# Optimization experiments

Measured on AMD Instinct MI355X. Metric: run time of the kernel, lower is better.

Reference implementation:

```python
import jax, jax.numpy as jnp
import numpy as np

N = 50000   # n_nodes (cells)
E = 800000  # n_edges (avg degree 16)
D = 128     # feature dim


def setup_inputs() -> dict:
    key = jax.random.key(0)
    ks = jax.random.split(key, 8)
    x = jax.random.normal(ks[0], (N, D), dtype=jnp.float32)
    src = jax.random.randint(ks[1], (E,), 0, N, dtype=jnp.int32)
    dst = jax.random.randint(ks[2], (E,), 0, N, dtype=jnp.int32)
    vals = jax.random.uniform(ks[3], (E,), dtype=jnp.float32)
    # GraphConvolution weight (dim -> dim), applied as x @ W
    W_gc = jax.random.normal(ks[4], (D, D), dtype=jnp.float32) / np.sqrt(D).astype(np.float32)
    b_gc = jnp.zeros((D,), jnp.float32)
    # linear2: nn.Linear(dim, dim) -> x @ W2.T + b2
    W2 = jax.random.normal(ks[5], (D, D), dtype=jnp.float32) / np.sqrt(D).astype(np.float32)
    b2 = jnp.zeros((D,), jnp.float32)
    return {"x": x, "vals": vals, "W_gc": W_gc, "b_gc": b_gc,
            "W2": W2, "b2": b2, "src": src, "dst": dst}


def reference(x, vals, W_gc, b_gc, W2, b2, src, dst):
    # GraphConvolution (dropout is identity in eval mode):
    #   support = x @ W + b ; out = relu(adj_sparse @ support)
    support = x @ W_gc + b_gc                         # [N, D]
    msg = support[src] * vals[:, None]                # gather rows, scale by edge weight
    agg = jax.ops.segment_sum(msg, dst, num_segments=N)  # SpMM via scatter-add
    x1 = jax.nn.relu(agg)                             # [N, D]
    # linear2 + dropout(eval=identity) + detached L2 row-normalize
    x2 = x1 @ W2.T + b2                               # [N, D]
    nrm = jax.lax.stop_gradient(
        jnp.sqrt(jnp.sum(x2 * x2, axis=1, keepdims=True)))
    return x2 / nrm
```

## Files before the change

### kernel.cpp

```cpp
#include <hip/hip_runtime.h>
#include <hip/hip_bf16.h>

#define N_NODES 50000
#define N_EDGES 800000
#define DIM     128
#define N_STRIPS (N_NODES / 16)
#define N_BKT    782
#define EDGE_CHUNKS 196
#define BCAP     1536
#define EBUF_CAP 1408
#define AGS      68
#define GEMM_BLOCKS ((N_STRIPS + 3) / 4)
#define FRONT_BLOCKS (GEMM_BLOCKS + EDGE_CHUNKS)

typedef short short8 __attribute__((ext_vector_type(8)));
typedef float floatx4 __attribute__((ext_vector_type(4)));

__device__ inline unsigned short f2bf(float f) {
    __hip_bfloat16 h = __float2bfloat16(f);
    return *reinterpret_cast<unsigned short*>(&h);
}

__global__ __launch_bounds__(256) void pre_pack(
    const float* __restrict__ W1, const float* __restrict__ W2,
    uint4* __restrict__ p1, uint4* __restrict__ p2, int* __restrict__ bcnt)
{
    const int blk = blockIdx.x;
    const int t   = threadIdx.x;
    if (blk < 8) {
        const int s    = blk * 256 + t;
        const int lane = s & 63;
        const int nt   = (s >> 6) & 7;
        const int ks   = s >> 9;
        const int m    = lane & 15;
        const int q    = lane >> 4;
        unsigned short e[8];
        #pragma unroll
        for (int j = 0; j < 8; ++j)
            e[j] = f2bf(W1[(ks * 32 + q * 8 + j) * DIM + nt * 16 + m]);
        uint4 o;
        o.x = (unsigned)e[0] | ((unsigned)e[1] << 16);
        o.y = (unsigned)e[2] | ((unsigned)e[3] << 16);
        o.z = (unsigned)e[4] | ((unsigned)e[5] << 16);
        o.w = (unsigned)e[6] | ((unsigned)e[7] << 16);
        p1[s] = o;
    } else if (blk < 16) {
        const int s    = (blk - 8) * 256 + t;
        const int lane = s & 63;
        const int nt   = (s >> 6) & 7;
        const int ks   = s >> 9;
        const int m    = lane & 15;
        const int q    = lane >> 4;
        const float4 f0 = *reinterpret_cast<const float4*>(&W2[(nt * 16 + m) * DIM + ks * 32 + q * 8]);
        const float4 f1 = *reinterpret_cast<const float4*>(&W2[(nt * 16 + m) * DIM + ks * 32 + q * 8 + 4]);
        unsigned short e[8];
        e[0] = f2bf(f0.x); e[1] = f2bf(f0.y); e[2] = f2bf(f0.z); e[3] = f2bf(f0.w);
        e[4] = f2bf(f1.x); e[5] = f2bf(f1.y); e[6] = f2bf(f1.z); e[7] = f2bf(f1.w);
        uint4 o;
        o.x = (unsigned)e[0] | ((unsigned)e[1] << 16);
        o.y = (unsigned)e[2] | ((unsigned)e[3] << 16);
        o.z = (unsigned)e[4] | ((unsigned)e[5] << 16);
        o.w = (unsigned)e[6] | ((unsigned)e[7] << 16);
        p2[s] = o;
    } else {
        for (int i = t; i < 800; i += 256) bcnt[i] = 0;
    }
}

__global__ __launch_bounds__(256) void front(
    const float* __restrict__ x, const float* __restrict__ bias,
    const int* __restrict__ src, const int* __restrict__ dst,
    const float* __restrict__ vals, const uint4* __restrict__ p1,
    unsigned short* __restrict__ support, int* __restrict__ bcnt,
    int2* __restrict__ bucketed)
{
    __shared__ int bh[800];
    __shared__ int rcur[800];
    const int t = threadIdx.x;

    if (blockIdx.x < EDGE_CHUNKS) {
        const int chunk = blockIdx.x;
        for (int i = t; i < 800; i += 256) bh[i] = 0;
        __syncthreads();
        const int base   = chunk * 4096;
        const int navail = min(4096, N_EDGES - base);
        const int4* d4 = reinterpret_cast<const int4*>(dst + base);
        #pragma unroll
        for (int i = 0; i < 4; ++i) {
            const int j = t + i * 256;
            if (j * 4 < navail) {
                const int4 d = d4[j];
                atomicAdd(&bh[d.x >> 6], 1);
                atomicAdd(&bh[d.y >> 6], 1);
                atomicAdd(&bh[d.z >> 6], 1);
                atomicAdd(&bh[d.w >> 6], 1);
            }
        }
        __syncthreads();
        for (int b = t; b < N_BKT; b += 256)
            rcur[b] = b * BCAP + atomicAdd(&bcnt[b], bh[b]);
        __syncthreads();
        const int4*   s4 = reinterpret_cast<const int4*>(src + base);
        const float4* v4 = reinterpret_cast<const float4*>(vals + base);
        #pragma unroll
        for (int i = 0; i < 4; ++i) {
            const int j = t + i * 256;
            if (j * 4 < navail) {
                const int4   s = s4[j];
                const int4   d = d4[j];
                const float4 v = v4[j];
                int p;
                p = atomicAdd(&rcur[d.x >> 6], 1);
                bucketed[p] = make_int2((s.x & 0xFFFF) | ((d.x & 63) << 16), __float_as_int(v.x));
                p = atomicAdd(&rcur[d.y >> 6], 1);
                bucketed[p] = make_int2((s.y & 0xFFFF) | ((d.y & 63) << 16), __float_as_int(v.y));
                p = atomicAdd(&rcur[d.z >> 6], 1);
                bucketed[p] = make_int2((s.z & 0xFFFF) | ((d.z & 63) << 16), __float_as_int(v.z));
                p = atomicAdd(&rcur[d.w >> 6], 1);
                bucketed[p] = make_int2((s.w & 0xFFFF) | ((d.w & 63) << 16), __float_as_int(v.w));
            }
        }
    } else {
        const int wave  = t >> 6;
        const int lane  = t & 63;
        const int strip = (blockIdx.x - EDGE_CHUNKS) * 4 + wave;
        if (strip >= N_STRIPS) return;
        const int m = lane & 15;
        const int q = lane >> 4;
        const int row = strip * 16 + m;

        short8 a[4];
        const float4* xr = reinterpret_cast<const float4*>(&x[(size_t)row * DIM]);
        #pragma unroll
        for (int ks = 0; ks < 4; ++ks) {
            const float4 f0 = xr[ks * 8 + q * 2];
            const float4 f1 = xr[ks * 8 + q * 2 + 1];
            short8 tt;
            tt[0] = (short)f2bf(f0.x); tt[1] = (short)f2bf(f0.y);
            tt[2] = (short)f2bf(f0.z); tt[3] = (short)f2bf(f0.w);
            tt[4] = (short)f2bf(f1.x); tt[5] = (short)f2bf(f1.y);
            tt[6] = (short)f2bf(f1.z); tt[7] = (short)f2bf(f1.w);
            a[ks] = tt;
        }

        floatx4 acc[8];
        #pragma unroll
        for (int nt = 0; nt < 8; ++nt) { acc[nt][0]=0.f; acc[nt][1]=0.f; acc[nt][2]=0.f; acc[nt][3]=0.f; }

        const short8* Bp = (const short8*)p1;
        #pragma unroll
        for (int ks = 0; ks < 4; ++ks) {
            #pragma unroll
            for (int nt = 0; nt < 8; ++nt) {
                const short8 bf = Bp[(ks * 8 + nt) * 64 + lane];
                acc[nt] = __builtin_amdgcn_mfma_f32_16x16x32_bf16(a[ks], bf, acc[nt], 0, 0, 0);
            }
        }

        #pragma unroll
        for (int nt = 0; nt < 8; ++nt) {
            const float bb = bias[nt * 16 + m];
            #pragma unroll
            for (int i = 0; i < 4; ++i) {
                const int r = strip * 16 + q * 4 + i;
                support[(size_t)r * DIM + nt * 16 + m] = f2bf(acc[nt][i] + bb);
            }
        }
    }
}

__global__ __launch_bounds__(256) void agg_gemm2(
    const unsigned int* __restrict__ sup, const int2* __restrict__ bucketed,
    const int* __restrict__ bcnt, const short8* __restrict__ Bp,
    const float* __restrict__ bias, float* __restrict__ out)
{
    __shared__ int2 ebuf[EBUF_CAP];
    __shared__ unsigned int agg[64 * AGS];
    __shared__ int cnt[64];
    __shared__ int coff[64];
    __shared__ int cur[64];

    const int b = blockIdx.x;
    const int t = threadIdx.x;
    int nE = bcnt[b];
    if (nE > EBUF_CAP) nE = EBUF_CAP;
    const int base = b * BCAP;

    if (t < 64) cnt[t] = 0;
    __syncthreads();
    for (int i = t; i < nE; i += 256)
        atomicAdd(&cnt[(bucketed[base + i].x >> 16) & 63], 1);
    __syncthreads();
    if (t < 64) coff[t] = cnt[t];
    __syncthreads();
    for (int off = 1; off < 64; off <<= 1) {
        int u = 0;
        if (t < 64 && t >= off) u = coff[t - off];
        __syncthreads();
        if (t < 64 && t >= off) coff[t] += u;
        __syncthreads();
    }
    if (t < 64) cur[t] = coff[t] - cnt[t];
    __syncthreads();
    for (int i = t; i < nE; i += 256) {
        const int2 e = bucketed[base + i];
        const int  n = (e.x >> 16) & 63;
        const int  p = atomicAdd(&cur[n], 1);
        ebuf[p] = e;
    }
    __syncthreads();

    const int w    = t >> 6;
    const int lane = t & 63;
    const int g    = lane >> 4;
    const int dl   = lane & 15;

    for (int nl = w * 16; nl < w * 16 + 16; ++nl) {
        const int end = cur[nl];
        const int c   = cnt[nl];
        const int beg = end - c;
        float acc[8];
        #pragma unroll
        for (int k = 0; k < 8; ++k) acc[k] = 0.f;

        const int nI = (c + 3) >> 2;
        auto step = [&](int it) {
            const int  idx = beg + it * 4 + g;
            const bool vld = idx < end;
            const int2 e   = ebuf[vld ? idx : beg];
            const float val = vld ? __int_as_float(e.y) : 0.f;
            const uint4 u = *reinterpret_cast<const uint4*>(
                &sup[(size_t)(e.x & 0xFFFF) * 64 + dl * 4]);
            acc[0] += __uint_as_float(u.x << 16)          * val;
            acc[1] += __uint_as_float(u.x & 0xffff0000u)  * val;
            acc[2] += __uint_as_float(u.y << 16)          * val;
            acc[3] += __uint_as_float(u.y & 0xffff0000u)  * val;
            acc[4] += __uint_as_float(u.z << 16)          * val;
            acc[5] += __uint_as_float(u.z & 0xffff0000u)  * val;
            acc[6] += __uint_as_float(u.w << 16)          * val;
            acc[7] += __uint_as_float(u.w & 0xffff0000u)  * val;
        };
        int it = 0;
        for (; it + 3 < nI; it += 4) { step(it); step(it+1); step(it+2); step(it+3); }
        for (; it < nI; ++it) step(it);

        #pragma unroll
        for (int k = 0; k < 8; ++k) {
            acc[k] += __shfl_xor(acc[k], 16);
            acc[k] += __shfl_xor(acc[k], 32);
        }
        if (dl == lane) {
            uint4 o;
            o.x = (unsigned)f2bf(fmaxf(acc[0],0.f)) | ((unsigned)f2bf(fmaxf(acc[1],0.f)) << 16);
            o.y = (unsigned)f2bf(fmaxf(acc[2],0.f)) | ((unsigned)f2bf(fmaxf(acc[3],0.f)) << 16);
            o.z = (unsigned)f2bf(fmaxf(acc[4],0.f)) | ((unsigned)f2bf(fmaxf(acc[5],0.f)) << 16);
            o.w = (unsigned)f2bf(fmaxf(acc[6],0.f)) | ((unsigned)f2bf(fmaxf(acc[7],0.f)) << 16);
            *reinterpret_cast<uint4*>(&agg[nl * AGS + dl * 4]) = o;
        }
    }
    __syncthreads();

    const int row0 = b * 64 + w * 16;
    if (row0 >= N_NODES) return;
    const int m = lane & 15;
    const int q = lane >> 4;

    short8 a[4];
    #pragma unroll
    for (int ks = 0; ks < 4; ++ks) {
        const uint4 t4 = *reinterpret_cast<const uint4*>(&agg[(w * 16 + m) * AGS + ks * 16 + q * 4]);
        a[ks] = *reinterpret_cast<const short8*>(&t4);
    }

    floatx4 acc[8];
    #pragma unroll
    for (int nt = 0; nt < 8; ++nt) { acc[nt][0]=0.f; acc[nt][1]=0.f; acc[nt][2]=0.f; acc[nt][3]=0.f; }

    #pragma unroll
    for (int ks = 0; ks < 4; ++ks) {
        #pragma unroll
        for (int nt = 0; nt < 8; ++nt) {
            const short8 bf = Bp[(ks * 8 + nt) * 64 + lane];
            acc[nt] = __builtin_amdgcn_mfma_f32_16x16x32_bf16(a[ks], bf, acc[nt], 0, 0, 0);
        }
    }

    #pragma unroll
    for (int nt = 0; nt < 8; ++nt) {
        const float bb = bias[nt * 16 + m];
        #pragma unroll
        for (int i = 0; i < 4; ++i) acc[nt][i] += bb;
    }

    float sq[4] = {0.f, 0.f, 0.f, 0.f};
    #pragma unroll
    for (int nt = 0; nt < 8; ++nt)
        #pragma unroll
        for (int i = 0; i < 4; ++i) sq[i] += acc[nt][i] * acc[nt][i];
    #pragma unroll
    for (int i = 0; i < 4; ++i) {
        #pragma unroll
        for (int mask = 1; mask < 16; mask <<= 1)
            sq[i] += __shfl_xor(sq[i], mask);
        sq[i] = 1.0f / sqrtf(sq[i]);
    }

    #pragma unroll
    for (int nt = 0; nt < 8; ++nt) {
        #pragma unroll
        for (int i = 0; i < 4; ++i) {
            const int r = row0 + q * 4 + i;
            out[(size_t)r * DIM + nt * 16 + m] = acc[nt][i] * sq[i];
        }
    }
}

extern "C" void kernel_launch(void* const* d_in, const int* in_sizes, int n_in,
                              void* d_out, int out_size, void* d_ws, size_t ws_size,
                              hipStream_t stream) {
    const float* x    = (const float*)d_in[0];
    const float* vals = (const float*)d_in[1];
    const float* W_gc = (const float*)d_in[2];
    const float* b_gc = (const float*)d_in[3];
    const float* W2   = (const float*)d_in[4];
    const float* b2   = (const float*)d_in[5];
    const int*   src  = (const int*)d_in[6];
    const int*   dst  = (const int*)d_in[7];

    float* out = (float*)d_out;

    const size_t SUP_B = (size_t)N_NODES * DIM * 2;
    const size_t BUK_B = (size_t)N_BKT * BCAP * 8;
    char* wsb = (char*)d_ws;
    unsigned short* support = (unsigned short*)wsb;
    int2* bucketed = (int2*)(wsb + SUP_B);
    int*  bcnt     = (int*)(wsb + SUP_B + BUK_B);
    uint4* pw1     = (uint4*)(wsb + SUP_B + BUK_B + 4096);
    uint4* pw2     = (uint4*)(wsb + SUP_B + BUK_B + 4096 + 32768);

    pre_pack<<<17, 256, 0, stream>>>(W_gc, W2, pw1, pw2, bcnt);

    front<<<FRONT_BLOCKS, 256, 0, stream>>>(
        x, b_gc, src, dst, vals, pw1, support, bcnt, bucketed);

    agg_gemm2<<<N_BKT, 256, 0, stream>>>(
        (const unsigned int*)support, bucketed, bcnt, (const short8*)pw2, b2, out);
}
```

Before: 148.4 us.

## Reorder to aggregate-then-transform, fusing both GEMMs into aggregation kernel

Uses associativity, A(xW+b) = (Ax)W + rowsum(A)·b. Aggregation now gathers bf16 copies of x directly and also tracks the per-node sum of edge weights, then applies the first GEMM (with bias scaled by that sum) and ReLU in the aggregation kernel before the second GEMM. The first kernel now only buckets edges, converts x to bf16 and packs the weights, instead of running GEMM1. The bucket-count zeroing moves to a memset, and the aggregation block grows to 512 threads, with only 4 of its 8 waves doing the GEMMs. This removes the separate GEMM1 pass and the support round trip, but adds a standalone x-to-bf16 conversion pass and leaves half the waves idle during the GEMM phase.

```diff
diff --git a/kernel.cpp b/kernel.cpp
--- a/kernel.cpp
+++ b/kernel.cpp
@@ -4,14 +4,14 @@
 #define N_NODES 50000
 #define N_EDGES 800000
 #define DIM     128
-#define N_STRIPS (N_NODES / 16)
 #define N_BKT    782
+#define CHUNK_E  4096
 #define EDGE_CHUNKS 196
 #define BCAP     1536
 #define EBUF_CAP 1408
+#define CONV_BLOCKS 128
+#define D1_BLOCKS (EDGE_CHUNKS + CONV_BLOCKS + 16)
 #define AGS      68
-#define GEMM_BLOCKS ((N_STRIPS + 3) / 4)
-#define FRONT_BLOCKS (GEMM_BLOCKS + EDGE_CHUNKS)
 
 typedef short short8 __attribute__((ext_vector_type(8)));
 typedef float floatx4 __attribute__((ext_vector_type(4)));
@@ -21,14 +21,84 @@
     return *reinterpret_cast<unsigned short*>(&h);
 }
 
-__global__ __launch_bounds__(256) void pre_pack(
-    const float* __restrict__ W1, const float* __restrict__ W2,
-    uint4* __restrict__ p1, uint4* __restrict__ p2, int* __restrict__ bcnt)
+__device__ inline uint4 pack8(const float a[8]) {
+    uint4 o;
+    o.x = (unsigned)f2bf(a[0]) | ((unsigned)f2bf(a[1]) << 16);
+    o.y = (unsigned)f2bf(a[2]) | ((unsigned)f2bf(a[3]) << 16);
+    o.z = (unsigned)f2bf(a[4]) | ((unsigned)f2bf(a[5]) << 16);
+    o.w = (unsigned)f2bf(a[6]) | ((unsigned)f2bf(a[7]) << 16);
+    return o;
+}
+
+__global__ __launch_bounds__(256) void fused1(
+    const float* __restrict__ x, const float* __restrict__ W1,
+    const float* __restrict__ W2,
+    const int* __restrict__ src, const int* __restrict__ dst,
+    const float* __restrict__ vals,
+    unsigned int* __restrict__ xb, int* __restrict__ bcnt,
+    int2* __restrict__ bucketed,
+    uint4* __restrict__ p1, uint4* __restrict__ p2)
 {
-    const int blk = blockIdx.x;
-    const int t   = threadIdx.x;
-    if (blk < 8) {
-        const int s    = blk * 256 + t;
+    __shared__ int bh[800];
+    __shared__ int rcur[800];
+    const int t = threadIdx.x;
+
+    if (blockIdx.x < EDGE_CHUNKS) {
+        const int chunk = blockIdx.x;
+        for (int i = t; i < 800; i += 256) bh[i] = 0;
+        __syncthreads();
+        const int base   = chunk * CHUNK_E;
+        const int navail = min(CHUNK_E, N_EDGES - base);
+        const int4* d4 = reinterpret_cast<const int4*>(dst + base);
+        #pragma unroll
+        for (int i = 0; i < 4; ++i) {
+            const int j = t + i * 256;
+            if (j * 4 < navail) {
+                const int4 d = d4[j];
+                atomicAdd(&bh[d.x >> 6], 1);
+                atomicAdd(&bh[d.y >> 6], 1);
+                atomicAdd(&bh[d.z >> 6], 1);
+                atomicAdd(&bh[d.w >> 6], 1);
+            }
+        }
+        __syncthreads();
+        for (int b = t; b < N_BKT; b += 256)
+            rcur[b] = b * BCAP + atomicAdd(&bcnt[b], bh[b]);
+        __syncthreads();
+        const int4*   s4 = reinterpret_cast<const int4*>(src + base);
+        const float4* v4 = reinterpret_cast<const float4*>(vals + base);
+        #pragma unroll
+        for (int i = 0; i < 4; ++i) {
+            const int j = t + i * 256;
+            if (j * 4 < navail) {
+                const int4   s = s4[j];
+                const int4   d = d4[j];
+                const float4 v = v4[j];
+                int p;
+                p = atomicAdd(&rcur[d.x >> 6], 1);
+                bucketed[p] = make_int2((s.x & 0xFFFF) | ((d.x & 63) << 16), __float_as_int(v.x));
+                p = atomicAdd(&rcur[d.y >> 6], 1);
+                bucketed[p] = make_int2((s.y & 0xFFFF) | ((d.y & 63) << 16), __float_as_int(v.y));
+                p = atomicAdd(&rcur[d.z >> 6], 1);
+                bucketed[p] = make_int2((s.z & 0xFFFF) | ((d.z & 63) << 16), __float_as_int(v.z));
+                p = atomicAdd(&rcur[d.w >> 6], 1);
+                bucketed[p] = make_int2((s.w & 0xFFFF) | ((d.w & 63) << 16), __float_as_int(v.w));
+            }
+        }
+    } else if (blockIdx.x < EDGE_CHUNKS + CONV_BLOCKS) {
+        const int cb = blockIdx.x - EDGE_CHUNKS;
+        const float4* x4 = reinterpret_cast<const float4*>(x);
+        uint2* xb2 = reinterpret_cast<uint2*>(xb);
+        for (int i = cb * 256 + t; i < N_NODES * DIM / 4; i += CONV_BLOCKS * 256) {
+            const float4 f = x4[i];
+            uint2 o;
+            o.x = (unsigned)f2bf(f.x) | ((unsigned)f2bf(f.y) << 16);
+            o.y = (unsigned)f2bf(f.z) | ((unsigned)f2bf(f.w) << 16);
+            xb2[i] = o;
+        }
+    } else if (blockIdx.x < EDGE_CHUNKS + CONV_BLOCKS + 8) {
+        const int pb   = blockIdx.x - (EDGE_CHUNKS + CONV_BLOCKS);
+        const int s    = pb * 256 + t;
         const int lane = s & 63;
         const int nt   = (s >> 6) & 7;
         const int ks   = s >> 9;
@@ -44,8 +114,9 @@
         o.z = (unsigned)e[4] | ((unsigned)e[5] << 16);
         o.w = (unsigned)e[6] | ((unsigned)e[7] << 16);
         p1[s] = o;
-    } else if (blk < 16) {
-        const int s    = (blk - 8) * 256 + t;
+    } else {
+        const int pb   = blockIdx.x - (EDGE_CHUNKS + CONV_BLOCKS + 8);
+        const int s    = pb * 256 + t;
         const int lane = s & 63;
         const int nt   = (s >> 6) & 7;
         const int ks   = s >> 9;
@@ -62,120 +133,19 @@
         o.z = (unsigned)e[4] | ((unsigned)e[5] << 16);
         o.w = (unsigned)e[6] | ((unsigned)e[7] << 16);
         p2[s] = o;
-    } else {
-        for (int i = t; i < 800; i += 256) bcnt[i] = 0;
-    }
-}
-
-__global__ __launch_bounds__(256) void front(
-    const float* __restrict__ x, const float* __restrict__ bias,
-    const int* __restrict__ src, const int* __restrict__ dst,
-    const float* __restrict__ vals, const uint4* __restrict__ p1,
-    unsigned short* __restrict__ support, int* __restrict__ bcnt,
-    int2* __restrict__ bucketed)
-{
-    __shared__ int bh[800];
-    __shared__ int rcur[800];
-    const int t = threadIdx.x;
-
-    if (blockIdx.x < EDGE_CHUNKS) {
-        const int chunk = blockIdx.x;
-        for (int i = t; i < 800; i += 256) bh[i] = 0;
-        __syncthreads();
-        const int base   = chunk * 4096;
-        const int navail = min(4096, N_EDGES - base);
-        const int4* d4 = reinterpret_cast<const int4*>(dst + base);
-        #pragma unroll
-        for (int i = 0; i < 4; ++i) {
-            const int j = t + i * 256;
-            if (j * 4 < navail) {
-                const int4 d = d4[j];
-                atomicAdd(&bh[d.x >> 6], 1);
-                atomicAdd(&bh[d.y >> 6], 1);
-                atomicAdd(&bh[d.z >> 6], 1);
-                atomicAdd(&bh[d.w >> 6], 1);
-            }
-        }
-        __syncthreads();
-        for (int b = t; b < N_BKT; b += 256)
-            rcur[b] = b * BCAP + atomicAdd(&bcnt[b], bh[b]);
-        __syncthreads();
-        const int4*   s4 = reinterpret_cast<const int4*>(src + base);
-        const float4* v4 = reinterpret_cast<const float4*>(vals + base);
-        #pragma unroll
-        for (int i = 0; i < 4; ++i) {
-            const int j = t + i * 256;
-            if (j * 4 < navail) {
-                const int4   s = s4[j];
-                const int4   d = d4[j];
-                const float4 v = v4[j];
-                int p;
-                p = atomicAdd(&rcur[d.x >> 6], 1);
-                bucketed[p] = make_int2((s.x & 0xFFFF) | ((d.x & 63) << 16), __float_as_int(v.x));
-                p = atomicAdd(&rcur[d.y >> 6], 1);
-                bucketed[p] = make_int2((s.y & 0xFFFF) | ((d.y & 63) << 16), __float_as_int(v.y));
-                p = atomicAdd(&rcur[d.z >> 6], 1);
-                bucketed[p] = make_int2((s.z & 0xFFFF) | ((d.z & 63) << 16), __float_as_int(v.z));
-                p = atomicAdd(&rcur[d.w >> 6], 1);
-                bucketed[p] = make_int2((s.w & 0xFFFF) | ((d.w & 63) << 16), __float_as_int(v.w));
-            }
-        }
-    } else {
-        const int wave  = t >> 6;
-        const int lane  = t & 63;
-        const int strip = (blockIdx.x - EDGE_CHUNKS) * 4 + wave;
-        if (strip >= N_STRIPS) return;
-        const int m = lane & 15;
-        const int q = lane >> 4;
-        const int row = strip * 16 + m;
-
-        short8 a[4];
-        const float4* xr = reinterpret_cast<const float4*>(&x[(size_t)row * DIM]);
-        #pragma unroll
-        for (int ks = 0; ks < 4; ++ks) {
-            const float4 f0 = xr[ks * 8 + q * 2];
-            const float4 f1 = xr[ks * 8 + q * 2 + 1];
-            short8 tt;
-            tt[0] = (short)f2bf(f0.x); tt[1] = (short)f2bf(f0.y);
-            tt[2] = (short)f2bf(f0.z); tt[3] = (short)f2bf(f0.w);
-            tt[4] = (short)f2bf(f1.x); tt[5] = (short)f2bf(f1.y);
-            tt[6] = (short)f2bf(f1.z); tt[7] = (short)f2bf(f1.w);
-            a[ks] = tt;
-        }
-
-        floatx4 acc[8];
-        #pragma unroll
-        for (int nt = 0; nt < 8; ++nt) { acc[nt][0]=0.f; acc[nt][1]=0.f; acc[nt][2]=0.f; acc[nt][3]=0.f; }
-
-        const short8* Bp = (const short8*)p1;
-        #pragma unroll
-        for (int ks = 0; ks < 4; ++ks) {
-            #pragma unroll
-            for (int nt = 0; nt < 8; ++nt) {
-                const short8 bf = Bp[(ks * 8 + nt) * 64 + lane];
-                acc[nt] = __builtin_amdgcn_mfma_f32_16x16x32_bf16(a[ks], bf, acc[nt], 0, 0, 0);
-            }
-        }
-
-        #pragma unroll
-        for (int nt = 0; nt < 8; ++nt) {
-            const float bb = bias[nt * 16 + m];
-            #pragma unroll
-            for (int i = 0; i < 4; ++i) {
-                const int r = strip * 16 + q * 4 + i;
-                support[(size_t)r * DIM + nt * 16 + m] = f2bf(acc[nt][i] + bb);
-            }
-        }
-    }
-}
-
-__global__ __launch_bounds__(256) void agg_gemm2(
-    const unsigned int* __restrict__ sup, const int2* __restrict__ bucketed,
-    const int* __restrict__ bcnt, const short8* __restrict__ Bp,
-    const float* __restrict__ bias, float* __restrict__ out)
+    }
+}
+
+__global__ __launch_bounds__(512) void agg_gemms(
+    const unsigned int* __restrict__ xb, const int2* __restrict__ bucketed,
+    const int* __restrict__ bcnt,
+    const short8* __restrict__ Bp1, const short8* __restrict__ Bp2,
+    const float* __restrict__ bias1, const float* __restrict__ bias2,
+    float* __restrict__ out)
 {
     __shared__ int2 ebuf[EBUF_CAP];
     __shared__ unsigned int agg[64 * AGS];
+    __shared__ float sv[64];
     __shared__ int cnt[64];
     __shared__ int coff[64];
     __shared__ int cur[64];
@@ -188,7 +158,7 @@
 
     if (t < 64) cnt[t] = 0;
     __syncthreads();
-    for (int i = t; i < nE; i += 256)
+    for (int i = t; i < nE; i += 512)
         atomicAdd(&cnt[(bucketed[base + i].x >> 16) & 63], 1);
     __syncthreads();
     if (t < 64) coff[t] = cnt[t];
@@ -202,7 +172,7 @@
     }
     if (t < 64) cur[t] = coff[t] - cnt[t];
     __syncthreads();
-    for (int i = t; i < nE; i += 256) {
+    for (int i = t; i < nE; i += 512) {
         const int2 e = bucketed[base + i];
         const int  n = (e.x >> 16) & 63;
         const int  p = atomicAdd(&cur[n], 1);
@@ -215,13 +185,14 @@
     const int g    = lane >> 4;
     const int dl   = lane & 15;
 
-    for (int nl = w * 16; nl < w * 16 + 16; ++nl) {
+    for (int nl = w * 8; nl < w * 8 + 8; ++nl) {
         const int end = cur[nl];
         const int c   = cnt[nl];
         const int beg = end - c;
         float acc[8];
         #pragma unroll
         for (int k = 0; k < 8; ++k) acc[k] = 0.f;
+        float sval = 0.f;
 
         const int nI = (c + 3) >> 2;
         auto step = [&](int it) {
@@ -230,7 +201,8 @@
             const int2 e   = ebuf[vld ? idx : beg];
             const float val = vld ? __int_as_float(e.y) : 0.f;
             const uint4 u = *reinterpret_cast<const uint4*>(
-                &sup[(size_t)(e.x & 0xFFFF) * 64 + dl * 4]);
+                &xb[(size_t)(e.x & 0xFFFF) * 64 + dl * 4]);
+            sval += val;
             acc[0] += __uint_as_float(u.x << 16)          * val;
             acc[1] += __uint_as_float(u.x & 0xffff0000u)  * val;
             acc[2] += __uint_as_float(u.y << 16)          * val;
@@ -249,26 +221,60 @@
             acc[k] += __shfl_xor(acc[k], 16);
             acc[k] += __shfl_xor(acc[k], 32);
         }
-        if (dl == lane) {
-            uint4 o;
-            o.x = (unsigned)f2bf(fmaxf(acc[0],0.f)) | ((unsigned)f2bf(fmaxf(acc[1],0.f)) << 16);
-            o.y = (unsigned)f2bf(fmaxf(acc[2],0.f)) | ((unsigned)f2bf(fmaxf(acc[3],0.f)) << 16);
-            o.z = (unsigned)f2bf(fmaxf(acc[4],0.f)) | ((unsigned)f2bf(fmaxf(acc[5],0.f)) << 16);
-            o.w = (unsigned)f2bf(fmaxf(acc[6],0.f)) | ((unsigned)f2bf(fmaxf(acc[7],0.f)) << 16);
-            *reinterpret_cast<uint4*>(&agg[nl * AGS + dl * 4]) = o;
-        }
-    }
-    __syncthreads();
-
-    const int row0 = b * 64 + w * 16;
-    if (row0 >= N_NODES) return;
+        sval += __shfl_xor(sval, 16);
+        sval += __shfl_xor(sval, 32);
+        if (lane == 0) sv[nl] = sval;
+        if (lane < 16) {
+            *reinterpret_cast<uint4*>(&agg[nl * AGS + dl * 4]) = pack8(acc);
+        }
+    }
+    __syncthreads();
+
+    const bool act = (w < 4) && (b * 64 + w * 16 < N_NODES);
     const int m = lane & 15;
     const int q = lane >> 4;
+    unsigned short* aggs = reinterpret_cast<unsigned short*>(agg);
+
+    if (act) {
+        short8 a[4];
+        #pragma unroll
+        for (int ks = 0; ks < 4; ++ks) {
+            const uint4 t4 = *reinterpret_cast<const uint4*>(&agg[(w * 16 + m) * AGS + ks * 16 + q * 4]);
+            a[ks] = *reinterpret_cast<const short8*>(&t4);
+        }
+        floatx4 acc[8];
+        #pragma unroll
+        for (int nt = 0; nt < 8; ++nt) { acc[nt][0]=0.f; acc[nt][1]=0.f; acc[nt][2]=0.f; acc[nt][3]=0.f; }
+        #pragma unroll
+        for (int ks = 0; ks < 4; ++ks) {
+            #pragma unroll
+            for (int nt = 0; nt < 8; ++nt) {
+                const short8 bf = Bp1[(ks * 8 + nt) * 64 + lane];
+                acc[nt] = __builtin_amdgcn_mfma_f32_16x16x32_bf16(a[ks], bf, acc[nt], 0, 0, 0);
+            }
+        }
+        float sv4[4];
+        #pragma unroll
+        for (int i = 0; i < 4; ++i) sv4[i] = sv[w * 16 + q * 4 + i];
+        #pragma unroll
+        for (int nt = 0; nt < 8; ++nt) {
+            const float bb = bias1[nt * 16 + m];
+            #pragma unroll
+            for (int i = 0; i < 4; ++i) {
+                const float v = fmaxf(acc[nt][i] + sv4[i] * bb, 0.f);
+                aggs[(w * 16 + q * 4 + i) * (AGS * 2) + nt * 16 + m] = f2bf(v);
+            }
+        }
+    }
+    __syncthreads();
+
+    if (!act) return;
+    const int row0 = b * 64 + w * 16;
 
     short8 a[4];
     #pragma unroll
     for (int ks = 0; ks < 4; ++ks) {
-        const uint4 t4 = *reinterpret_cast<const uint4*>(&agg[(w * 16 + m) * AGS + ks * 16 + q * 4]);
+        const uint4 t4 = *reinterpret_cast<const uint4*>(&aggs[(w * 16 + m) * (AGS * 2) + ks * 32 + q * 8]);
         a[ks] = *reinterpret_cast<const short8*>(&t4);
     }
 
@@ -280,14 +286,14 @@
     for (int ks = 0; ks < 4; ++ks) {
         #pragma unroll
         for (int nt = 0; nt < 8; ++nt) {
-            const short8 bf = Bp[(ks * 8 + nt) * 64 + lane];
+            const short8 bf = Bp2[(ks * 8 + nt) * 64 + lane];
             acc[nt] = __builtin_amdgcn_mfma_f32_16x16x32_bf16(a[ks], bf, acc[nt], 0, 0, 0);
         }
     }
 
     #pragma unroll
     for (int nt = 0; nt < 8; ++nt) {
-        const float bb = bias[nt * 16 + m];
+        const float bb = bias2[nt * 16 + m];
         #pragma unroll
         for (int i = 0; i < 4; ++i) acc[nt][i] += bb;
     }
@@ -329,20 +335,21 @@
 
     float* out = (float*)d_out;
 
-    const size_t SUP_B = (size_t)N_NODES * DIM * 2;
+    const size_t XB_B  = (size_t)N_NODES * DIM * 2;
     const size_t BUK_B = (size_t)N_BKT * BCAP * 8;
     char* wsb = (char*)d_ws;
-    unsigned short* support = (unsigned short*)wsb;
-    int2* bucketed = (int2*)(wsb + SUP_B);
-    int*  bcnt     = (int*)(wsb + SUP_B + BUK_B);
-    uint4* pw1     = (uint4*)(wsb + SUP_B + BUK_B + 4096);
-    uint4* pw2     = (uint4*)(wsb + SUP_B + BUK_B + 4096 + 32768);
-
-    pre_pack<<<17, 256, 0, stream>>>(W_gc, W2, pw1, pw2, bcnt);
-
-    front<<<FRONT_BLOCKS, 256, 0, stream>>>(
-        x, b_gc, src, dst, vals, pw1, support, bcnt, bucketed);
-
-    agg_gemm2<<<N_BKT, 256, 0, stream>>>(
-        (const unsigned int*)support, bucketed, bcnt, (const short8*)pw2, b2, out);
-}
+    unsigned int* xb = (unsigned int*)wsb;
+    int2*  bucketed = (int2*)(wsb + XB_B);
+    int*   bcnt     = (int*)(wsb + XB_B + BUK_B);
+    uint4* pw1      = (uint4*)(wsb + XB_B + BUK_B + 4096);
+    uint4* pw2      = (uint4*)(wsb + XB_B + BUK_B + 4096 + 32768);
+
+    hipMemsetAsync(bcnt, 0, 800 * sizeof(int), stream);
+
+    fused1<<<D1_BLOCKS, 256, 0, stream>>>(
+        x, W_gc, W2, src, dst, vals, xb, bcnt, bucketed, pw1, pw2);
+
+    agg_gemms<<<N_BKT, 512, 0, stream>>>(
+        xb, bucketed, bcnt, (const short8*)pw1, (const short8*)pw2,
+        b_gc, b2, out);
+}
```

New measurement: 153.7 us. +3.6%, slower.
